# Kernel tuning notes

Measured on AMD Instinct MI355X. Metric: run time of the kernel, lower is better.

The kernel has to match this reference:

```python
import jax, jax.numpy as jnp
import numpy as np

ITERATIONS = 3

def setup_inputs() -> dict:
    key = jax.random.key(0)
    k1, k2 = jax.random.split(key)
    C, S, H = 64, 128, 2048
    x = jax.random.normal(k1, (C, S, H), dtype=jnp.float32)
    W = jax.random.normal(k2, (H, H), dtype=jnp.float32)
    return {"x": x, "W": W}

def reference(x, W):
    # x: [C, S, H], W: [H, H]
    C, S, H = x.shape
    # e_ij is loop-invariant in the original; hoist it (same math, computed once)
    e_ij = jnp.einsum('csh,hk->csk', x, W)  # [C, S, H]
    b_ij = jnp.zeros((C, S), dtype=x.dtype)
    c_i = jnp.zeros((C, H), dtype=x.dtype)
    for _ in range(ITERATIONS):
        d_i = jax.nn.softmax(b_ij, axis=1)[:, :, None]          # [C, S, 1], softmax over S
        c_i = jnp.sum(d_i * e_ij, axis=1)                        # [C, H]
        squared = jnp.sum(c_i ** 2, axis=1, keepdims=True)       # [C, 1]
        coeff = squared / (1.0 + squared) / jnp.sqrt(squared + 1e-9)
        c_i = coeff * c_i                                        # squash
        b_ij = b_ij + jnp.einsum('csh,ch->cs', e_ij, c_i)        # logit update
    return c_i
```

## Files before the change

kernel.cpp:

```cpp
#include <hip/hip_runtime.h>

using bf16x8 = __attribute__((ext_vector_type(8))) __bf16;
using f32x4  = __attribute__((ext_vector_type(4))) float;

#define C_ 64
#define S_ 128
#define H_ 2048
#define M_ 8192

__device__ __forceinline__ unsigned short f2bf(float f) {
  unsigned u = __float_as_uint(f);
  u = u + 0x7fffu + ((u >> 16) & 1u);
  return (unsigned short)(u >> 16);
}
__device__ __forceinline__ float bf2f(unsigned short h) {
  return __uint_as_float(((unsigned)h) << 16);
}

__device__ __forceinline__ void glds16(const unsigned short* g, unsigned short* l) {
  __builtin_amdgcn_global_load_lds(
      (const __attribute__((address_space(1))) void*)g,
      (__attribute__((address_space(3))) void*)l, 16, 0, 0);
}

__global__ void k_split_all(const float* __restrict__ x,
                            unsigned short* __restrict__ xh,
                            unsigned short* __restrict__ xl,
                            const float* __restrict__ W,
                            unsigned short* __restrict__ Wth,
                            unsigned short* __restrict__ Wtl,
                            float* __restrict__ G) {
  __shared__ float Ts[64][68];
  const int b = blockIdx.x;
  const int t = threadIdx.x;
  if (b < 16384) {
    int idx = b * 256 + t;
    float4 v = ((const float4*)x)[idx];
    float a[4] = {v.x, v.y, v.z, v.w};
    unsigned short h[4], l[4];
#pragma unroll
    for (int q = 0; q < 4; ++q) {
      h[q] = f2bf(a[q]);
      l[q] = f2bf(a[q] - bf2f(h[q]));
    }
    ((ushort4*)xh)[idx] = make_ushort4(h[0], h[1], h[2], h[3]);
    ((ushort4*)xl)[idx] = make_ushort4(l[0], l[1], l[2], l[3]);
  } else if (b < 17408) {
    const int bb = b - 16384;
    const int k0 = (bb & 31) * 64, n0 = (bb >> 5) * 64;
#pragma unroll
    for (int p = 0; p < 4; ++p) {
      int idx = t + p * 256;
      int r = idx >> 4, c4 = (idx & 15) * 4;
      *(float4*)&Ts[r][c4] = *(const float4*)(W + (size_t)(k0 + r) * H_ + n0 + c4);
    }
    __syncthreads();
#pragma unroll
    for (int p = 0; p < 4; ++p) {
      int idx = t + p * 256;
      int rr = idx >> 4, cc = (idx & 15) * 4;
      unsigned short h[4], l[4];
#pragma unroll
      for (int q = 0; q < 4; ++q) {
        float f = Ts[cc + q][rr];
        h[q] = f2bf(f);
        l[q] = f2bf(f - bf2f(h[q]));
      }
      size_t o = (size_t)(n0 + rr) * H_ + k0 + cc;
      *(ushort4*)(Wth + o) = make_ushort4(h[0], h[1], h[2], h[3]);
      *(ushort4*)(Wtl + o) = make_ushort4(l[0], l[1], l[2], l[3]);
    }
  } else {
    const int bb = b - 17408;
    ((float4*)G)[bb * 256 + t] = (float4){0.f, 0.f, 0.f, 0.f};
  }
}

#define TILE_USH 24576
#define OFF_AH 0
#define OFF_AL 8192
#define OFF_BH 16384
#define OFF_BL 20480

#define DSREAD(dst, addr, OFFLIT) \
  asm volatile("ds_read_b128 %0, %1 offset:" OFFLIT : "=v"(dst) : "v"(addr))

#define MF3(I, J, CAH, CAL, CBH, CBL)                                                          \
  acc[I][J] = __builtin_amdgcn_mfma_f32_16x16x32_bf16(CAH[I], CBH[J], acc[I][J], 0, 0, 0);     \
  acc[I][J] = __builtin_amdgcn_mfma_f32_16x16x32_bf16(CAH[I], CBL[J], acc[I][J], 0, 0, 0);     \
  acc[I][J] = __builtin_amdgcn_mfma_f32_16x16x32_bf16(CAL[I], CBH[J], acc[I][J], 0, 0, 0);

#define SB __builtin_amdgcn_sched_barrier(0)

#define TILE_ILV(RAH, RAL, RBH, RBL, CAH, CAL, CBH, CBL, off_ush)        \
  do {                                                                   \
    const unsigned _ab = aAb + (unsigned)(off_ush) * 2u;                 \
    const unsigned _bb = aBb + (unsigned)(off_ush) * 2u;                 \
    __builtin_amdgcn_s_setprio(1);                                       \
    DSREAD(RAH[0], _ab, "0");     DSREAD(RAH[1], _ab, "1024");     SB;   \
    MF3(0, 0, CAH, CAL, CBH, CBL) MF3(0, 1, CAH, CAL, CBH, CBL)    SB;   \
    DSREAD(RAH[2], _ab, "2048");  DSREAD(RAH[3], _ab, "3072");     SB;   \
    MF3(0, 2, CAH, CAL, CBH, CBL) MF3(0, 3, CAH, CAL, CBH, CBL)    SB;   \
    DSREAD(RAL[0], _ab, "16384"); DSREAD(RAL[1], _ab, "17408");    SB;   \
    MF3(1, 0, CAH, CAL, CBH, CBL) MF3(1, 1, CAH, CAL, CBH, CBL)    SB;   \
    DSREAD(RAL[2], _ab, "18432"); DSREAD(RAL[3], _ab, "19456");    SB;   \
    MF3(1, 2, CAH, CAL, CBH, CBL) MF3(1, 3, CAH, CAL, CBH, CBL)    SB;   \
    DSREAD(RBH[0], _bb, "32768"); DSREAD(RBH[1], _bb, "33792");    SB;   \
    MF3(2, 0, CAH, CAL, CBH, CBL) MF3(2, 1, CAH, CAL, CBH, CBL)    SB;   \
    DSREAD(RBH[2], _bb, "34816"); DSREAD(RBH[3], _bb, "35840");    SB;   \
    MF3(2, 2, CAH, CAL, CBH, CBL) MF3(2, 3, CAH, CAL, CBH, CBL)    SB;   \
    DSREAD(RBL[0], _bb, "40960"); DSREAD(RBL[1], _bb, "41984");    SB;   \
    MF3(3, 0, CAH, CAL, CBH, CBL) MF3(3, 1, CAH, CAL, CBH, CBL)    SB;   \
    DSREAD(RBL[2], _bb, "43008"); DSREAD(RBL[3], _bb, "44032");    SB;   \
    MF3(3, 2, CAH, CAL, CBH, CBL) MF3(3, 3, CAH, CAL, CBH, CBL)    SB;   \
    __builtin_amdgcn_s_setprio(0);                                       \
  } while (0)

#define LOADSET_ASM(AH, AL, BH, BL, off_ush)                      \
  do {                                                            \
    unsigned _ab = aAb + (unsigned)(off_ush) * 2u;                \
    unsigned _bb = aBb + (unsigned)(off_ush) * 2u;                \
    DSREAD(AH[0], _ab, "0");     DSREAD(AH[1], _ab, "1024");      \
    DSREAD(AH[2], _ab, "2048");  DSREAD(AH[3], _ab, "3072");      \
    DSREAD(AL[0], _ab, "16384"); DSREAD(AL[1], _ab, "17408");     \
    DSREAD(AL[2], _ab, "18432"); DSREAD(AL[3], _ab, "19456");     \
    DSREAD(BH[0], _bb, "32768"); DSREAD(BH[1], _bb, "33792");     \
    DSREAD(BH[2], _bb, "34816"); DSREAD(BH[3], _bb, "35840");     \
    DSREAD(BL[0], _bb, "40960"); DSREAD(BL[1], _bb, "41984");     \
    DSREAD(BL[2], _bb, "43008"); DSREAD(BL[3], _bb, "44032");     \
  } while (0)

#define MFMASET(AH, AL, BH, BL)                                                                  \
  do {                                                                                           \
    __builtin_amdgcn_s_setprio(1);                                                               \
    _Pragma("unroll") for (int i = 0; i < 4; ++i)                                                \
        _Pragma("unroll") for (int j = 0; j < 4; ++j) {                                          \
      acc[i][j] = __builtin_amdgcn_mfma_f32_16x16x32_bf16(AH[i], BH[j], acc[i][j], 0, 0, 0);     \
      acc[i][j] = __builtin_amdgcn_mfma_f32_16x16x32_bf16(AH[i], BL[j], acc[i][j], 0, 0, 0);     \
      acc[i][j] = __builtin_amdgcn_mfma_f32_16x16x32_bf16(AL[i], BH[j], acc[i][j], 0, 0, 0);     \
    }                                                                                            \
    __builtin_amdgcn_s_setprio(0);                                                               \
  } while (0)

__global__ __launch_bounds__(512, 2) void k_gemm3(
    const unsigned short* __restrict__ Ah, const unsigned short* __restrict__ Al,
    const unsigned short* __restrict__ Bh, const unsigned short* __restrict__ Bl,
    unsigned short* __restrict__ Eh, unsigned short* __restrict__ El) {
  __shared__ unsigned short lds[3 * TILE_USH];
  const int t = threadIdx.x;
  const int lane = t & 63, wid = t >> 6;
  const int wm = wid >> 1, wn = wid & 1;
  const int l16 = lane & 15, quad = lane >> 4;

  const int lin = blockIdx.x + (blockIdx.y << 5);
  const int xcd = lin & 7, slot = lin >> 3;
  const int bm = ((xcd >> 1) << 3) + (slot >> 3);
  const int bn = ((xcd & 1) << 3) + (slot & 7);

  const int rl = lane >> 2;
  const int gg8 = (((lane & 3) ^ ((rl >> 1) & 3)) << 3);
  const unsigned short* gAh0 = Ah + (size_t)(bm * 256 + wid * 16 + rl) * H_ + gg8;
  const unsigned short* gAl0 = Al + (size_t)(bm * 256 + wid * 16 + rl) * H_ + gg8;
  const unsigned short* gAh1 = gAh0 + (size_t)128 * H_;
  const unsigned short* gAl1 = gAl0 + (size_t)128 * H_;
  const unsigned short* gBh  = Bh + (size_t)(bn * 128 + wid * 16 + rl) * H_ + gg8;
  const unsigned short* gBl  = Bl + (size_t)(bn * 128 + wid * 16 + rl) * H_ + gg8;
  const int dA0 = wid * 512;
  const int dA1 = dA0 + 4096;
  const int dB  = wid * 512;

  const int colq = ((quad ^ ((l16 >> 1) & 3)) << 3);
  const int rA = (wm * 64 + l16) * 32 + colq;
  const int rB = (wn * 64 + l16) * 32 + colq;
  const unsigned ldsb = (unsigned)(uintptr_t)&lds[0];
  const unsigned aAb = ldsb + (unsigned)rA * 2u;
  const unsigned aBb = ldsb + (unsigned)rB * 2u;

  f32x4 acc[4][4];
#pragma unroll
  for (int i = 0; i < 4; ++i)
#pragma unroll
    for (int j = 0; j < 4; ++j) acc[i][j] = (f32x4)0.f;

  auto stage6 = [&](int bo, int k) {
    glds16(gAh0 + k, &lds[bo + OFF_AH + dA0]);
    glds16(gAh1 + k, &lds[bo + OFF_AH + dA1]);
    glds16(gAl0 + k, &lds[bo + OFF_AL + dA0]);
    glds16(gAl1 + k, &lds[bo + OFF_AL + dA1]);
    glds16(gBh + k,  &lds[bo + OFF_BH + dB]);
    glds16(gBl + k,  &lds[bo + OFF_BL + dB]);
  };

  stage6(0, 0);
  stage6(TILE_USH, 32);
  asm volatile("s_waitcnt vmcnt(6)" ::: "memory");
  __builtin_amdgcn_s_barrier();
  __builtin_amdgcn_sched_barrier(0);

  bf16x8 ahA[4], alA[4], bhA[4], blA[4];
  bf16x8 ahB[4], alB[4], bhB[4], blB[4];
  LOADSET_ASM(ahA, alA, bhA, blA, 0);

  int stage_off = 2 * TILE_USH;
  int read_off  = TILE_USH;

#pragma unroll 1
  for (int tt = 0; tt < 62; tt += 2) {
    stage6(stage_off, (tt + 2) * 32);
    stage_off += TILE_USH; if (stage_off == 3 * TILE_USH) stage_off = 0;
    asm volatile("s_waitcnt vmcnt(6) lgkmcnt(0)" ::: "memory");
    __builtin_amdgcn_s_barrier();
    __builtin_amdgcn_sched_barrier(0);
    TILE_ILV(ahB, alB, bhB, blB, ahA, alA, bhA, blA, read_off);
    read_off += TILE_USH; if (read_off == 3 * TILE_USH) read_off = 0;
    stage6(stage_off, (tt + 3) * 32);
    stage_off += TILE_USH; if (stage_off == 3 * TILE_USH) stage_off = 0;
    asm volatile("s_waitcnt vmcnt(6) lgkmcnt(0)" ::: "memory");
    __builtin_amdgcn_s_barrier();
    __builtin_amdgcn_sched_barrier(0);
    TILE_ILV(ahA, alA, bhA, blA, ahB, alB, bhB, blB, read_off);
    read_off += TILE_USH; if (read_off == 3 * TILE_USH) read_off = 0;
  }

  asm volatile("s_waitcnt vmcnt(0) lgkmcnt(0)" ::: "memory");
  __builtin_amdgcn_s_barrier();
  __builtin_amdgcn_sched_barrier(0);
  LOADSET_ASM(ahB, alB, bhB, blB, read_off);
  __builtin_amdgcn_sched_barrier(0);
  MFMASET(ahA, alA, bhA, blA);
  asm volatile("s_waitcnt lgkmcnt(0)" ::: "memory");
  __builtin_amdgcn_sched_barrier(0);
  MFMASET(ahB, alB, bhB, blB);

#pragma unroll
  for (int i = 0; i < 4; ++i) {
    const int row0 = bm * 256 + wm * 64 + i * 16 + quad * 4;
#pragma unroll
    for (int j = 0; j < 4; ++j) {
      const int col = bn * 128 + wn * 64 + j * 16 + l16;
#pragma unroll
      for (int r = 0; r < 4; ++r) {
        float v = acc[i][j][r];
        unsigned short hh = f2bf(v);
        unsigned short ll = f2bf(v - bf2f(hh));
        Eh[(size_t)(row0 + r) * H_ + col] = hh;
        El[(size_t)(row0 + r) * H_ + col] = ll;
      }
    }
  }
}

__global__ __launch_bounds__(256, 4) void k_gram_mfma(
    const unsigned short* __restrict__ Eh, const unsigned short* __restrict__ El,
    float* __restrict__ G) {
  __shared__ unsigned short sb[2][16384];
  const int t = threadIdx.x;
  const int kc = blockIdx.x;
  const int cc = blockIdx.y;
  const int lane = t & 63, wid = t >> 6;
  const int wm = wid >> 1, wn = wid & 1;
  const int l16 = lane & 15, quad = lane >> 4;

  const int rl = lane >> 2;
  const int gg = (lane & 3) ^ ((rl >> 1) & 3);
  const int c0 = wid * 2, c1 = c0 + 1;
  const unsigned short* gH0 = Eh + (size_t)(cc * 128 + c0 * 16 + rl) * H_ + gg * 8;
  const unsigned short* gH1 = Eh + (size_t)(cc * 128 + c1 * 16 + rl) * H_ + gg * 8;
  const unsigned short* gL0 = El + (size_t)(cc * 128 + c0 * 16 + rl) * H_ + gg * 8;
  const unsigned short* gL1 = El + (size_t)(cc * 128 + c1 * 16 + rl) * H_ + gg * 8;
  const int dH0 = c0 * 512, dH1 = c1 * 512;

  const int swz = ((l16 >> 1) & 3);
  const int colq = ((quad ^ swz) * 8);

  f32x4 acc[4][4];
#pragma unroll
  for (int i = 0; i < 4; ++i)
#pragma unroll
    for (int j = 0; j < 4; ++j) acc[i][j] = (f32x4)0.f;

  auto stage4 = [&](int buf, int k) {
    glds16(gH0 + k, &sb[buf][dH0]);
    glds16(gH1 + k, &sb[buf][dH1]);
    glds16(gL0 + k, &sb[buf][8192 + dH0]);
    glds16(gL1 + k, &sb[buf][8192 + dH1]);
  };

  const int kbeg = kc * 256;
  stage4(0, kbeg);
  asm volatile("s_waitcnt vmcnt(0)" ::: "memory");
  __builtin_amdgcn_s_barrier();

  int cur = 0;
#pragma unroll 1
  for (int s = 0; s < 8; ++s) {
    if (s < 7) stage4(cur ^ 1, kbeg + (s + 1) * 32);
    const unsigned short* sH = &sb[cur][0];
    const unsigned short* sL = &sb[cur][8192];
    bf16x8 ah[4], al[4], bh[4], bl[4];
#pragma unroll
    for (int i = 0; i < 4; ++i) {
      const int ra = (wm * 64 + i * 16 + l16) * 32;
      const int rb = (wn * 64 + i * 16 + l16) * 32;
      ah[i] = *(const bf16x8*)&sH[ra + colq];
      al[i] = *(const bf16x8*)&sL[ra + colq];
      bh[i] = *(const bf16x8*)&sH[rb + colq];
      bl[i] = *(const bf16x8*)&sL[rb + colq];
    }
    __builtin_amdgcn_s_setprio(1);
#pragma unroll
    for (int i = 0; i < 4; ++i)
#pragma unroll
      for (int j = 0; j < 4; ++j) {
        acc[i][j] = __builtin_amdgcn_mfma_f32_16x16x32_bf16(ah[i], bh[j], acc[i][j], 0, 0, 0);
        acc[i][j] = __builtin_amdgcn_mfma_f32_16x16x32_bf16(ah[i], bl[j], acc[i][j], 0, 0, 0);
        acc[i][j] = __builtin_amdgcn_mfma_f32_16x16x32_bf16(al[i], bh[j], acc[i][j], 0, 0, 0);
      }
    __builtin_amdgcn_s_setprio(0);
    if (s < 7) {
      asm volatile("s_waitcnt vmcnt(0) lgkmcnt(0)" ::: "memory");
      __builtin_amdgcn_s_barrier();
    }
    cur ^= 1;
  }

  float* Gc = G + (size_t)cc * S_ * S_;
#pragma unroll
  for (int i = 0; i < 4; ++i) {
    const int row0 = wm * 64 + i * 16 + quad * 4;
#pragma unroll
    for (int j = 0; j < 4; ++j) {
      const int col = wn * 64 + j * 16 + l16;
#pragma unroll
      for (int r = 0; r < 4; ++r)
        atomicAdd(&Gc[(row0 + r) * S_ + col], acc[i][j][r]);
    }
  }
}

__global__ void k_out2(const unsigned short* __restrict__ Eh,
                       const unsigned short* __restrict__ El,
                       const float* __restrict__ G, float* __restrict__ out) {
  const int c = blockIdx.y;
  const int s = threadIdx.x & 127;
  __shared__ float dsh[128];
  __shared__ float red[128];
  __shared__ float wsh[128];
  const float* Gc = G + (size_t)c * S_ * S_;
  float b = 0.f;
  for (int it = 0; it < 3; ++it) {
    red[s] = b; __syncthreads();
    for (int off = 64; off > 0; off >>= 1) {
      if (s < off) red[s] = fmaxf(red[s], red[s + off]);
      __syncthreads();
    }
    float mx = red[0]; __syncthreads();
    float ev = expf(b - mx);
    red[s] = ev; __syncthreads();
    for (int off = 64; off > 0; off >>= 1) {
      if (s < off) red[s] = red[s] + red[s + off];
      __syncthreads();
    }
    float Z = red[0]; __syncthreads();
    float d = ev / Z;
    dsh[s] = d; __syncthreads();
    float y = 0.f;
#pragma unroll 8
    for (int j = 0; j < S_; ++j) y = fmaf(Gc[j * S_ + s], dsh[j], y);
    red[s] = d * y; __syncthreads();
    for (int off = 64; off > 0; off >>= 1) {
      if (s < off) red[s] = red[s] + red[s + off];
      __syncthreads();
    }
    float sq = red[0]; __syncthreads();
    float coeff = sq / (1.f + sq) / sqrtf(sq + 1e-9f);
    if (it == 2) wsh[s] = coeff * d;
    else b += coeff * y;
  }
  __syncthreads();

  const int h2 = blockIdx.x * 256 + threadIdx.x;
  const unsigned* Ph = (const unsigned*)(Eh + (size_t)c * S_ * H_) + h2;
  const unsigned* Pl = (const unsigned*)(El + (size_t)c * S_ * H_) + h2;
  float a0 = 0.f, a1 = 0.f;
#pragma unroll 8
  for (int ss = 0; ss < S_; ++ss) {
    unsigned uh = Ph[(size_t)ss * (H_ / 2)];
    unsigned ul = Pl[(size_t)ss * (H_ / 2)];
    a0 = fmaf(wsh[ss], bf2f((unsigned short)uh) + bf2f((unsigned short)ul), a0);
    a1 = fmaf(wsh[ss], bf2f((unsigned short)(uh >> 16)) + bf2f((unsigned short)(ul >> 16)), a1);
  }
  ((float2*)(out + (size_t)c * H_))[h2] = make_float2(a0, a1);
}

extern "C" void kernel_launch(void* const* d_in, const int* in_sizes, int n_in,
                              void* d_out, int out_size, void* d_ws, size_t ws_size,
                              hipStream_t stream) {
  (void)in_sizes; (void)n_in; (void)out_size; (void)ws_size;
  const float* x = (const float*)d_in[0];
  const float* W = (const float*)d_in[1];
  float* out = (float*)d_out;
  char* ws = (char*)d_ws;

  unsigned short* xh  = (unsigned short*)(ws);
  unsigned short* xl  = (unsigned short*)(ws + 33554432);
  unsigned short* Wth = (unsigned short*)(ws + 67108864);
  unsigned short* Wtl = (unsigned short*)(ws + 75497472);
  unsigned short* Eh  = (unsigned short*)(ws + 83886080);
  unsigned short* El  = (unsigned short*)(ws + 117440512);
  float*          G   = (float*)(ws + 150994944);

  k_split_all<<<dim3(18432), 256, 0, stream>>>(x, xh, xl, W, Wth, Wtl, G);
  k_gemm3<<<dim3(32, 16), 512, 0, stream>>>(xh, xl, Wth, Wtl, Eh, El);
  k_gram_mfma<<<dim3(8, 64), 256, 0, stream>>>(Eh, El, G);
  k_out2<<<dim3(4, 64), 256, 0, stream>>>(Eh, El, G, out);
}
```

Measured before the change: 348.0 us.

## Replace Gram atomics with per-split partial buffers reduced into LDS

```diff
diff --git a/kernel.cpp b/kernel.cpp
--- a/kernel.cpp
+++ b/kernel.cpp
@@ -28,8 +28,7 @@
                             unsigned short* __restrict__ xl,
                             const float* __restrict__ W,
                             unsigned short* __restrict__ Wth,
-                            unsigned short* __restrict__ Wtl,
-                            float* __restrict__ G) {
+                            unsigned short* __restrict__ Wtl) {
   __shared__ float Ts[64][68];
   const int b = blockIdx.x;
   const int t = threadIdx.x;
@@ -45,7 +44,7 @@
     }
     ((ushort4*)xh)[idx] = make_ushort4(h[0], h[1], h[2], h[3]);
     ((ushort4*)xl)[idx] = make_ushort4(l[0], l[1], l[2], l[3]);
-  } else if (b < 17408) {
+  } else {
     const int bb = b - 16384;
     const int k0 = (bb & 31) * 64, n0 = (bb >> 5) * 64;
 #pragma unroll
@@ -70,9 +69,6 @@
       *(ushort4*)(Wth + o) = make_ushort4(h[0], h[1], h[2], h[3]);
       *(ushort4*)(Wtl + o) = make_ushort4(l[0], l[1], l[2], l[3]);
     }
-  } else {
-    const int bb = b - 17408;
-    ((float4*)G)[bb * 256 + t] = (float4){0.f, 0.f, 0.f, 0.f};
   }
 }
 
@@ -252,7 +248,7 @@
 
 __global__ __launch_bounds__(256, 4) void k_gram_mfma(
     const unsigned short* __restrict__ Eh, const unsigned short* __restrict__ El,
-    float* __restrict__ G) {
+    float* __restrict__ G4) {
   __shared__ unsigned short sb[2][16384];
   const int t = threadIdx.x;
   const int kc = blockIdx.x;
@@ -286,15 +282,15 @@
     glds16(gL1 + k, &sb[buf][8192 + dH1]);
   };
 
-  const int kbeg = kc * 256;
+  const int kbeg = kc * 512;
   stage4(0, kbeg);
   asm volatile("s_waitcnt vmcnt(0)" ::: "memory");
   __builtin_amdgcn_s_barrier();
 
   int cur = 0;
 #pragma unroll 1
-  for (int s = 0; s < 8; ++s) {
-    if (s < 7) stage4(cur ^ 1, kbeg + (s + 1) * 32);
+  for (int s = 0; s < 16; ++s) {
+    if (s < 15) stage4(cur ^ 1, kbeg + (s + 1) * 32);
     const unsigned short* sH = &sb[cur][0];
     const unsigned short* sL = &sb[cur][8192];
     bf16x8 ah[4], al[4], bh[4], bl[4];
@@ -317,14 +313,14 @@
         acc[i][j] = __builtin_amdgcn_mfma_f32_16x16x32_bf16(al[i], bh[j], acc[i][j], 0, 0, 0);
       }
     __builtin_amdgcn_s_setprio(0);
-    if (s < 7) {
+    if (s < 15) {
       asm volatile("s_waitcnt vmcnt(0) lgkmcnt(0)" ::: "memory");
       __builtin_amdgcn_s_barrier();
     }
     cur ^= 1;
   }
 
-  float* Gc = G + (size_t)cc * S_ * S_;
+  float* Gp = G4 + ((size_t)(kc * 64 + cc)) * (S_ * S_);
 #pragma unroll
   for (int i = 0; i < 4; ++i) {
     const int row0 = wm * 64 + i * 16 + quad * 4;
@@ -333,20 +329,33 @@
       const int col = wn * 64 + j * 16 + l16;
 #pragma unroll
       for (int r = 0; r < 4; ++r)
-        atomicAdd(&Gc[(row0 + r) * S_ + col], acc[i][j][r]);
+        Gp[(row0 + r) * S_ + col] = acc[i][j][r];
     }
   }
 }
 
 __global__ void k_out2(const unsigned short* __restrict__ Eh,
                        const unsigned short* __restrict__ El,
-                       const float* __restrict__ G, float* __restrict__ out) {
+                       const float* __restrict__ G4, float* __restrict__ out) {
   const int c = blockIdx.y;
-  const int s = threadIdx.x & 127;
+  const int t = threadIdx.x;
+  const int s = t & 127;
+  __shared__ float Gl[128 * 128];
   __shared__ float dsh[128];
   __shared__ float red[128];
   __shared__ float wsh[128];
-  const float* Gc = G + (size_t)c * S_ * S_;
+
+  {
+    const float* g0 = G4 + ((size_t)(0 * 64 + c)) * 16384;
+    const float* g1 = G4 + ((size_t)(1 * 64 + c)) * 16384;
+    const float* g2 = G4 + ((size_t)(2 * 64 + c)) * 16384;
+    const float* g3 = G4 + ((size_t)(3 * 64 + c)) * 16384;
+#pragma unroll 8
+    for (int e = t; e < 16384; e += 256)
+      Gl[e] = (g0[e] + g1[e]) + (g2[e] + g3[e]);
+  }
+  __syncthreads();
+
   float b = 0.f;
   for (int it = 0; it < 3; ++it) {
     red[s] = b; __syncthreads();
@@ -364,9 +373,15 @@
     float Z = red[0]; __syncthreads();
     float d = ev / Z;
     dsh[s] = d; __syncthreads();
-    float y = 0.f;
+    float y0 = 0.f, y1 = 0.f, y2 = 0.f, y3 = 0.f;
 #pragma unroll 8
-    for (int j = 0; j < S_; ++j) y = fmaf(Gc[j * S_ + s], dsh[j], y);
+    for (int j = 0; j < S_; j += 4) {
+      y0 = fmaf(Gl[(j + 0) * S_ + s], dsh[j + 0], y0);
+      y1 = fmaf(Gl[(j + 1) * S_ + s], dsh[j + 1], y1);
+      y2 = fmaf(Gl[(j + 2) * S_ + s], dsh[j + 2], y2);
+      y3 = fmaf(Gl[(j + 3) * S_ + s], dsh[j + 3], y3);
+    }
+    float y = (y0 + y1) + (y2 + y3);
     red[s] = d * y; __syncthreads();
     for (int off = 64; off > 0; off >>= 1) {
       if (s < off) red[s] = red[s] + red[s + off];
@@ -408,10 +423,10 @@
   unsigned short* Wtl = (unsigned short*)(ws + 75497472);
   unsigned short* Eh  = (unsigned short*)(ws + 83886080);
   unsigned short* El  = (unsigned short*)(ws + 117440512);
-  float*          G   = (float*)(ws + 150994944);
-
-  k_split_all<<<dim3(18432), 256, 0, stream>>>(x, xh, xl, W, Wth, Wtl, G);
+  float*          G4  = (float*)(ws);
+
+  k_split_all<<<dim3(17408), 256, 0, stream>>>(x, xh, xl, W, Wth, Wtl);
   k_gemm3<<<dim3(32, 16), 512, 0, stream>>>(xh, xl, Wth, Wtl, Eh, El);
-  k_gram_mfma<<<dim3(8, 64), 256, 0, stream>>>(Eh, El, G);
-  k_out2<<<dim3(4, 64), 256, 0, stream>>>(Eh, El, G, out);
-}
+  k_gram_mfma<<<dim3(4, 64), 256, 0, stream>>>(Eh, El, G4);
+  k_out2<<<dim3(4, 64), 256, 0, stream>>>(Eh, El, G4, out);
+}
```

New measurement: 321.1 us. 1.08x faster.
